# Optimization experiments

Measured on AMD Instinct MI355X. Metric: run time of the kernel, lower is better.

## Reference

```python
import jax, jax.numpy as jnp
import numpy as np
import math

K = 1.0          # Lorentz manifold curvature param: points satisfy <x,x>_L = -K
NUM_HEADS = 16
EPS = 1e-6
B, L, D = 2, 2048, 1024


def lorentz_inner(x, y):
    # <x,y>_L = -x0*y0 + sum_{i>0} xi*yi  (over last dim)
    return jnp.sum(x * y, axis=-1) - 2.0 * x[..., 0] * y[..., 0]


def project_to_lorentz(z):
    # treat z[...,1:] as space components, recompute time so <x,x>_L = -K
    space = z[..., 1:]
    time = jnp.sqrt(K + jnp.sum(space * space, axis=-1, keepdims=True))
    return jnp.concatenate([time, space], axis=-1)


def hlinear(x, W, b, num_heads):
    # Lorentz linear layer (Chen et al. 2022): Euclidean affine map on the
    # ambient coordinates followed by curvature-aware time re-normalization.
    z = x @ W.T + b  # (B, L, D)
    if num_heads > 0:
        Bz, Lz, Dz = z.shape
        z = z.reshape(Bz, Lz, num_heads, Dz // num_heads)  # (B, L, H, dh)
    return project_to_lorentz(z)


def setup_inputs() -> dict:
    key = jax.random.key(0)
    ks = jax.random.split(key, 8)
    def mk_point(k):
        # random manifold points: random space part, valid time coordinate
        z = jax.random.normal(k, (B, L, D), dtype=jnp.float32) * 0.5
        return project_to_lorentz(z)
    scale = 1.0 / math.sqrt(D)
    def mk_w(k):
        return jax.random.normal(k, (D, D), dtype=jnp.float32) * scale
    return {
        "query": mk_point(ks[0]),
        "key": mk_point(ks[1]),
        "value": mk_point(ks[2]),
        "W_Q": mk_w(ks[3]), "b_Q": jnp.zeros((D,), jnp.float32),
        "W_K": mk_w(ks[4]), "b_K": jnp.zeros((D,), jnp.float32),
        "W_V": mk_w(ks[5]), "b_V": jnp.zeros((D,), jnp.float32),
        "W_O": mk_w(ks[6]), "b_O": jnp.zeros((D,), jnp.float32),
    }


def reference(query, key, value, W_Q, b_Q, W_K, b_K, W_V, b_V, W_O, b_O):
    H = NUM_HEADS
    q = hlinear(query, W_Q, b_Q, H)  # (B, L, H, dh) on per-head Lorentz manifold
    k = hlinear(key, W_K, b_K, H)
    v = hlinear(value, W_V, b_V, H)
    dh = q.shape[-1]
    # Lorentzian inner products <q_i, k_j>_L per head: (B, H, Lq, Lk)
    ip = (jnp.einsum('bqhd,bkhd->bhqk', q, k)
          - 2.0 * jnp.einsum('bqh,bkh->bhqk', q[..., 0], k[..., 0]))
    # negative squared Lorentz distance: -d_L^2 = 2K + 2<q,k>_L, scaled by sqrt(dh)
    scores = (2.0 * K + 2.0 * ip) * (1.0 / math.sqrt(dh))
    attn = jax.nn.softmax(scores, axis=-1)
    # Lorentzian centroid aggregation (Law et al.): normalize weighted sum back
    # onto the hyperboloid.
    mu = jnp.einsum('bhqk,bkhd->bqhd', attn, v)  # (B, L, H, dh)
    norm = jnp.sqrt(jnp.maximum(jnp.abs(lorentz_inner(mu, mu)), EPS))
    out_heads = math.sqrt(K) * mu / norm[..., None]
    cat = out_heads.reshape(out_heads.shape[0], out_heads.shape[1], -1)  # (B, L, D)
    return hlinear(cat, W_O, b_O, 0)  # (B, L, D) on the manifold
```

## Files before the change

kernel.cpp:

```cpp
#include <hip/hip_runtime.h>
#include <math.h>

namespace {
constexpr int Ln = 2048;
constexpr int Dn = 1024;
constexpr int Mn = 4096;
constexpr float QSCALE = 0.25f * 1.44269504088896340736f;
}

typedef unsigned short u16;
typedef unsigned int u32;
typedef __attribute__((ext_vector_type(4))) float f32x4;
typedef __attribute__((ext_vector_type(8))) __bf16 bf16x8;
typedef __attribute__((ext_vector_type(4))) unsigned short u16x4;
typedef __attribute__((ext_vector_type(8))) unsigned short u16x8;
typedef __attribute__((ext_vector_type(4))) unsigned int u32x4;


__device__ __forceinline__ u16 f2bf(float f) {
    union { float f; unsigned u; } cv; cv.f = f;
    unsigned u = cv.u + 0x7fffu + ((cv.u >> 16) & 1u);
    return (u16)(u >> 16);
}
__device__ __forceinline__ float bf2f(u16 h) {
    union { unsigned u; float f; } cv; cv.u = ((unsigned)h) << 16;
    return cv.f;
}

__device__ __forceinline__ u32 pkbf(float a, float b) {
    union { __bf16 h[2]; u32 u; } cv;
    cv.h[0] = (__bf16)a; cv.h[1] = (__bf16)b;
    return cv.u;
}

#if __has_builtin(__builtin_amdgcn_exp2f)
__device__ __forceinline__ float exp2_fast(float x) {
    return __builtin_amdgcn_exp2f(x);
}
#else
__device__ __forceinline__ float exp2_fast(float x) {
    float r;
    asm("v_exp_f32 %0, %1" : "=v"(r) : "v"(x));
    return r;
}
#endif

template <int CTRL>
__device__ __forceinline__ float dppf(float x) {
    return __int_as_float(__builtin_amdgcn_update_dpp(
        0, __float_as_int(x), CTRL, 0xf, 0xf, true));
}
__device__ __forceinline__ float red16_add(float x) {
    x += dppf<0xB1>(x);
    x += dppf<0x4E>(x);
    x += dppf<0x141>(x);
    x += dppf<0x140>(x);
    return x;
}

__device__ __forceinline__ void gload16(const void* g, void* l) {
    __builtin_amdgcn_global_load_lds(
        (const __attribute__((address_space(1))) unsigned int*)g,
        (__attribute__((address_space(3))) unsigned int*)l, 16, 0, 0);
}

__global__ __launch_bounds__(256)
void cvt_in3(const float* __restrict__ i0, const float* __restrict__ i1,
             const float* __restrict__ i2,
             u16* __restrict__ o0, u16* __restrict__ o1, u16* __restrict__ o2)
{
    const int z = blockIdx.y;
    const float* in = z == 0 ? i0 : (z == 1 ? i1 : i2);
    u16* out       = z == 0 ? o0 : (z == 1 ? o1 : o2);
    int i = blockIdx.x * 256 + threadIdx.x;
    f32x4 v = ((const f32x4*)in)[i];
    u16x4 o;
#pragma unroll
    for (int j = 0; j < 4; ++j) o[j] = f2bf(v[j]);
    int l = i >> 8;
    int e = (i & 255) * 4;
    int idx = l * 1024 + (e & ~63) + (((((e >> 3) & 7) ^ (l & 7))) << 3) + (e & 7);
    *(u16x4*)&out[idx] = o;
}

__global__ __launch_bounds__(256)
void cvt_w(const float* __restrict__ w0, const float* __restrict__ w1,
           const float* __restrict__ w2, const float* __restrict__ w3,
           u16* __restrict__ q0, u16* __restrict__ q1,
           u16* __restrict__ q2, u16* __restrict__ q3)
{
    const int z = blockIdx.y;
    int i = blockIdx.x * 256 + threadIdx.x;
    if (z < 3) {
        const float* in = z == 0 ? w0 : (z == 1 ? w1 : w2);
        u16* out       = z == 0 ? q0 : (z == 1 ? q1 : q2);
        f32x4 v = ((const f32x4*)in)[i];
        u16x4 o;
#pragma unroll
        for (int j = 0; j < 4; ++j) o[j] = f2bf(v[j]);
        int l = i >> 8;
        int e = (i & 255) * 4;
        int idx = l * 1024 + (e & ~63) + (((((e >> 3) & 7) ^ (l & 7))) << 3) + (e & 7);
        *(u16x4*)&out[idx] = o;
    } else {
        int o  = i >> 8;
        int s0 = (i & 255) * 4;
        int h = s0 >> 6, sl = s0 & 63, a = sl >> 2;
        const float* src = w3 + (size_t)o * 1024 + h * 64;
        u16x4 ov = { f2bf(src[a]), f2bf(src[16 + a]),
                     f2bf(src[32 + a]), f2bf(src[48 + a]) };
        int idx = o * 1024 + h * 64 + (((sl >> 3) ^ (o & 7)) << 3) + (sl & 7);
        *(u16x4*)&q3[idx] = ov;
    }
}

__global__ __launch_bounds__(256)
void gemm_qkv(const u16* __restrict__ xq, const u16* __restrict__ xk,
              const u16* __restrict__ xv, const u16* __restrict__ wq,
              const u16* __restrict__ wk, const u16* __restrict__ wv,
              const float* __restrict__ bq, const float* __restrict__ bk,
              const float* __restrict__ bv,
              u16* __restrict__ oq, u16* __restrict__ ok, u16* __restrict__ ov)
{
    __shared__ u16 As[2][64 * 64];
    __shared__ u16 Bs[2][128 * 64];
    const int t = threadIdx.x;
    const int lane = t & 63, w = t >> 6;
    const int g = lane >> 4, c = lane & 15;
    const int wr = w >> 1, wc = w & 1;
    const int id = blockIdx.x;
    const int bm = ((id & 7) * 8 + ((id >> 3) & 7)) * 64;
    const int bn = ((id >> 6) & 7) * 128;
    const int z  = id >> 9;

    const u16* A = z == 0 ? xq : (z == 1 ? xk : xv);
    const u16* W = z == 0 ? wq : (z == 1 ? wk : wv);
    const float* bias = z == 0 ? bq : (z == 1 ? bk : bv);
    u16* Ct = z == 0 ? oq : (z == 1 ? ok : ov);
    const float scale = z == 0 ? QSCALE : 1.f;
    const float tsign = z == 0 ? -1.f : 1.f;

    f32x4 acc[2][4];
    const f32x4 z4 = {0.f, 0.f, 0.f, 0.f};
#pragma unroll
    for (int i = 0; i < 2; ++i)
#pragma unroll
        for (int j = 0; j < 4; ++j) acc[i][j] = z4;

    const int sr = t >> 3, sb2 = (t & 7) * 8;
    const u16* Ap = A + (size_t)(bm + sr) * Dn + sb2;
    const u16* Wp = W + (size_t)(bn + sr) * Dn + sb2;

    auto stage = [&](int buf, int k0) {
        gload16(Ap + k0,            &As[buf][t * 8]);
        gload16(Ap + 32 * Dn + k0,  &As[buf][(256 + t) * 8]);
        gload16(Wp + k0,            &Bs[buf][t * 8]);
        gload16(Wp + 32 * Dn + k0,  &Bs[buf][(256 + t) * 8]);
        gload16(Wp + 64 * Dn + k0,  &Bs[buf][(512 + t) * 8]);
        gload16(Wp + 96 * Dn + k0,  &Bs[buf][(768 + t) * 8]);
    };

    stage(0, 0);
    for (int ki = 0; ki < 16; ++ki) {
        __syncthreads();
        if (ki + 1 < 16) stage((ki + 1) & 1, (ki + 1) * 64);
        const u16* as = As[ki & 1];
        const u16* bs = Bs[ki & 1];
#pragma unroll
        for (int kk = 0; kk < 2; ++kk) {
            const int so = ((kk * 4 + g) ^ (c & 7)) << 3;
            bf16x8 a[2], b[4];
#pragma unroll
            for (int mi = 0; mi < 2; ++mi)
                a[mi] = *(const bf16x8*)&as[(wr * 32 + mi * 16 + c) * 64 + so];
#pragma unroll
            for (int ni = 0; ni < 4; ++ni)
                b[ni] = *(const bf16x8*)&bs[(wc * 64 + ni * 16 + c) * 64 + so];
            __builtin_amdgcn_s_setprio(1);
#pragma unroll
            for (int mi = 0; mi < 2; ++mi)
#pragma unroll
                for (int ni = 0; ni < 4; ++ni)
                    acc[mi][ni] = __builtin_amdgcn_mfma_f32_16x16x32_bf16(
                        a[mi], b[ni], acc[mi][ni], 0, 0, 0);
            __builtin_amdgcn_s_setprio(0);
        }
    }

    const int hcb = bn + wc * 64;
    const int h = hcb >> 6;
#pragma unroll
    for (int mi = 0; mi < 2; ++mi)
#pragma unroll
        for (int j = 0; j < 4; ++j) {
            int ll = bm + wr * 32 + mi * 16 + g * 4 + j;
            float zv[4];
#pragma unroll
            for (int ni = 0; ni < 4; ++ni)
                zv[ni] = acc[mi][ni][j] + bias[hcb + ni * 16 + c];
            float loc = zv[0]*zv[0] + zv[1]*zv[1] + zv[2]*zv[2] + zv[3]*zv[3];
            if (c == 0) loc -= zv[0] * zv[0];
            loc = red16_add(loc);
            float tval = sqrtf(1.f + loc);
            float v0 = (c == 0) ? tsign * tval : zv[0];
            int bb = ll >> 11, l2 = ll & 2047;
            u16* dst = Ct + (((size_t)bb * 16 + h) * Ln + l2) * 64;
            u16x4 pkv = { f2bf(v0 * scale), f2bf(zv[1] * scale),
                          f2bf(zv[2] * scale), f2bf(zv[3] * scale) };
            *(u16x4*)&dst[(4 * c) ^ ((ll & 7) << 3)] = pkv;
        }
}

__global__ __launch_bounds__(256)
void transpose_v(const u16* __restrict__ vin, u16* __restrict__ vout)
{
    __shared__ u16 raw[64 * 64];
    const int t = threadIdx.x;
    const int bh = blockIdx.x, lc = blockIdx.y;
    const u16* src = vin + ((size_t)bh * Ln + lc * 64) * 64;
#pragma unroll
    for (int p = 0; p < 2; ++p) {
        int ci = p * 256 + t;
        *(u16x8*)&raw[ci * 8] = *(const u16x8*)(src + ci * 8);
    }
    __syncthreads();
    const int d = t >> 2, cp0 = (t & 3) * 16;
    const int s = ((d & 15) << 2) | (d >> 4);
    u16 buf[16];
#pragma unroll
    for (int i = 0; i < 16; ++i) {
        int cp = cp0 + i;
        int n = ((cp >> 5) << 5) | (((cp >> 2) & 1) << 4) | (((cp >> 3) & 3) << 2) | (cp & 3);
        buf[i] = raw[n * 64 + ((((s >> 3) ^ (n & 7)) << 3) | (s & 7))];
    }
    u16* dst = vout + ((size_t)bh * 64 + d) * Ln + lc * 64;
    int b0 = cp0 >> 3;
    *(u16x8*)&dst[((b0 ^ (d & 7)) << 3)]       = *(const u16x8*)&buf[0];
    *(u16x8*)&dst[(((b0 + 1) ^ (d & 7)) << 3)] = *(const u16x8*)&buf[8];
}

__global__ __launch_bounds__(256, 4)
void attn_mfma(const u16* __restrict__ qt, const u16* __restrict__ kt,
               const u16* __restrict__ vT, u16* __restrict__ part)
{
    __shared__ u16 smem[4 * 4096];

    const int t = threadIdx.x;
    const int lane = t & 63, w = t >> 6;
    const int g = lane >> 4, c = lane & 15;
    const int id  = blockIdx.x;
    const int qb  = (id >> 3) & 15;
    const int gidx = (id & 7) | ((id >> 7) << 3);
    const int bh  = gidx & 31;
    const int kvh = gidx >> 5;
    const int q0  = qb * 128;
    const u16* Q = qt + (size_t)bh * Ln * 64;
    const u16* K = kt + (size_t)bh * Ln * 64 + (size_t)kvh * (1024 * 64);
    const u16* V = vT + (size_t)bh * 64 * (size_t)Ln + kvh * 1024;

    bf16x8 qa[2][2];
#pragma unroll
    for (int mi = 0; mi < 2; ++mi)
#pragma unroll
        for (int kk = 0; kk < 2; ++kk) {
            int row = q0 + w * 32 + mi * 16 + c;
            qa[mi][kk] = *(const bf16x8*)(Q + (size_t)row * 64 +
                                          (((kk * 4 + g) ^ (c & 7)) << 3));
        }

    f32x4 o[2][4];
    const f32x4 z4 = {0.f, 0.f, 0.f, 0.f};
#pragma unroll
    for (int mi = 0; mi < 2; ++mi)
#pragma unroll
        for (int di = 0; di < 4; ++di) o[mi][di] = z4;

    const int fb0 = c * 128 + (((0 + g) ^ (c & 7)) << 4);
    const int fb1 = c * 128 + (((4 + g) ^ (c & 7)) << 4);

    char* sb = (char*)smem;
    const int cr = t >> 3, cb = t & 7;
    const u16* kp = K + (size_t)cr * 64 + cb * 8;
    const u16* vp = V + (size_t)cr * Ln + cb * 8;

    gload16(kp,            sb + t * 16);
    gload16(kp + 2048,     sb + 4096 + t * 16);
    gload16(vp,            sb + 16384 + t * 16);
    gload16(vp + 32 * Ln,  sb + 16384 + 4096 + t * 16);

    constexpr int NC = 1024 / 64;
    for (int ch = 0; ch < NC; ++ch) {
        __syncthreads();
        if (ch + 1 < NC) {
            const u16* kn = kp + (ch + 1) * 4096;
            const u16* vn = vp + (ch + 1) * 64;
            char* db = sb + (((ch + 1) & 1) << 13);
            gload16(kn,           db + t * 16);
            gload16(kn + 2048,    db + 4096 + t * 16);
            gload16(vn,           db + 16384 + t * 16);
            gload16(vn + 32 * Ln, db + 16384 + 4096 + t * 16);
        }
        const char* kbb = sb + ((ch & 1) << 13);
        const char* vbb = kbb + 16384;

        f32x4 sf[2][4];
#pragma unroll
        for (int mi = 0; mi < 2; ++mi)
#pragma unroll
            for (int ni = 0; ni < 4; ++ni) sf[mi][ni] = z4;
        __builtin_amdgcn_s_setprio(1);
#pragma unroll
        for (int kk = 0; kk < 2; ++kk) {
            const int fb = kk ? fb1 : fb0;
            bf16x8 kb[4];
#pragma unroll
            for (int ni = 0; ni < 4; ++ni)
                kb[ni] = *(const bf16x8*)(kbb + fb + ni * 2048);
#pragma unroll
            for (int mi = 0; mi < 2; ++mi)
#pragma unroll
                for (int ni = 0; ni < 4; ++ni)
                    sf[mi][ni] = __builtin_amdgcn_mfma_f32_16x16x32_bf16(
                        kb[ni], qa[mi][kk], sf[mi][ni], 0, 0, 0);
        }
        __builtin_amdgcn_s_setprio(0);

        bf16x8 paf[2][2];
#pragma unroll
        for (int mi = 0; mi < 2; ++mi) {
            float ex[4][4];
#pragma unroll
            for (int ni = 0; ni < 4; ++ni)
#pragma unroll
                for (int j = 0; j < 4; ++j)
                    ex[ni][j] = exp2_fast(sf[mi][ni][j]);
            u32x4 p0 = { pkbf(ex[0][0], ex[0][1]), pkbf(ex[0][2], ex[0][3]),
                         pkbf(ex[1][0], ex[1][1]), pkbf(ex[1][2], ex[1][3]) };
            u32x4 p1 = { pkbf(ex[2][0], ex[2][1]), pkbf(ex[2][2], ex[2][3]),
                         pkbf(ex[3][0], ex[3][1]), pkbf(ex[3][2], ex[3][3]) };
            paf[mi][0] = __builtin_bit_cast(bf16x8, p0);
            paf[mi][1] = __builtin_bit_cast(bf16x8, p1);
        }

        __builtin_amdgcn_s_setprio(1);
#pragma unroll
        for (int kk = 0; kk < 2; ++kk) {
            const int fb = kk ? fb1 : fb0;
#pragma unroll
            for (int di = 0; di < 4; ++di) {
                bf16x8 vb = *(const bf16x8*)(vbb + fb + di * 2048);
#pragma unroll
                for (int mi = 0; mi < 2; ++mi)
                    o[mi][di] = __builtin_amdgcn_mfma_f32_16x16x32_bf16(
                        paf[mi][kk], vb, o[mi][di], 0, 0, 0);
            }
        }
        __builtin_amdgcn_s_setprio(0);
    }

    u16* P = part + (size_t)(kvh * 32 + bh) * (4 * 2048 * 16);
#pragma unroll
    for (int mi = 0; mi < 2; ++mi)
#pragma unroll
        for (int j = 0; j < 4; ++j) {
            int row = q0 + w * 32 + mi * 16 + g * 4 + j;
#pragma unroll
            for (int di = 0; di < 4; ++di)
                P[(di * 2048 + row) * 16 + c] = f2bf(o[mi][di][j]);
        }
}

__global__ __launch_bounds__(256)
void attn_combine(const u16* __restrict__ part, u16* __restrict__ cat)
{
    const int grp = blockIdx.x * 16 + (threadIdx.x >> 4);
    const int c = threadIdx.x & 15;
    const int bh = grp >> 11, q = grp & 2047;
    const u16* P0 = part + (size_t)bh * (4 * 2048 * 16);
    const u16* P1 = part + (size_t)(32 + bh) * (4 * 2048 * 16);
    float mu[4];
#pragma unroll
    for (int di = 0; di < 4; ++di) {
        int idx = (di * 2048 + q) * 16 + c;
        mu[di] = bf2f(P0[idx]) + bf2f(P1[idx]);
    }
    float loc = mu[0]*mu[0] + mu[1]*mu[1] + mu[2]*mu[2] + mu[3]*mu[3];
    if (c == 0) loc -= 2.f * mu[0] * mu[0];
    loc = red16_add(loc);
    float rn = rsqrtf(fmaxf(fabsf(loc), 1e-6f));
    const int b = bh >> 4, h = bh & 15;
    u16* dst = cat + ((size_t)b * Ln + q) * Dn + h * 64;
    u16x4 pkv = { f2bf(mu[0] * rn), f2bf(mu[1] * rn),
                  f2bf(mu[2] * rn), f2bf(mu[3] * rn) };
    *(u16x4*)&dst[(4 * c) ^ ((q & 7) << 3)] = pkv;
}

__global__ __launch_bounds__(256)
void gemm_o(const u16* __restrict__ A, const u16* __restrict__ B,
            const float* __restrict__ bias, float* __restrict__ C)
{
    __shared__ u16 As[2][64 * 64];
    __shared__ u16 Bs[2][128 * 64];
    const int t = threadIdx.x;
    const int lane = t & 63, w = t >> 6;
    const int g = lane >> 4, c = lane & 15;
    const int wr = w >> 1, wc = w & 1;
    const int id = blockIdx.x;
    const int bm = ((id & 7) * 8 + ((id >> 3) & 7)) * 64;
    const int bn = (id >> 6) * 128;

    f32x4 acc[2][4];
    const f32x4 z4 = {0.f, 0.f, 0.f, 0.f};
#pragma unroll
    for (int i = 0; i < 2; ++i)
#pragma unroll
        for (int j = 0; j < 4; ++j) acc[i][j] = z4;

    const int sr = t >> 3, sb2 = (t & 7) * 8;
    const u16* Ap = A + (size_t)(bm + sr) * Dn + sb2;
    const u16* Bp = B + (size_t)(bn + sr) * Dn + sb2;

    auto stage = [&](int buf, int k0) {
        gload16(Ap + k0,            &As[buf][t * 8]);
        gload16(Ap + 32 * Dn + k0,  &As[buf][(256 + t) * 8]);
        gload16(Bp + k0,            &Bs[buf][t * 8]);
        gload16(Bp + 32 * Dn + k0,  &Bs[buf][(256 + t) * 8]);
        gload16(Bp + 64 * Dn + k0,  &Bs[buf][(512 + t) * 8]);
        gload16(Bp + 96 * Dn + k0,  &Bs[buf][(768 + t) * 8]);
    };

    stage(0, 0);
    for (int ki = 0; ki < 16; ++ki) {
        __syncthreads();
        if (ki + 1 < 16) stage((ki + 1) & 1, (ki + 1) * 64);
        const u16* as = As[ki & 1];
        const u16* bs = Bs[ki & 1];
#pragma unroll
        for (int kk = 0; kk < 2; ++kk) {
            const int so = ((kk * 4 + g) ^ (c & 7)) << 3;
            bf16x8 a[2], b[4];
#pragma unroll
            for (int mi = 0; mi < 2; ++mi)
                a[mi] = *(const bf16x8*)&as[(wr * 32 + mi * 16 + c) * 64 + so];
#pragma unroll
            for (int ni = 0; ni < 4; ++ni)
                b[ni] = *(const bf16x8*)&bs[(wc * 64 + ni * 16 + c) * 64 + so];
            __builtin_amdgcn_s_setprio(1);
#pragma unroll
            for (int mi = 0; mi < 2; ++mi)
#pragma unroll
                for (int ni = 0; ni < 4; ++ni)
                    acc[mi][ni] = __builtin_amdgcn_mfma_f32_16x16x32_bf16(
                        a[mi], b[ni], acc[mi][ni], 0, 0, 0);
            __builtin_amdgcn_s_setprio(0);
        }
    }

#pragma unroll
    for (int mi = 0; mi < 2; ++mi)
#pragma unroll
        for (int j = 0; j < 4; ++j) {
            size_t row = bm + wr * 32 + mi * 16 + g * 4 + j;
#pragma unroll
            for (int ni = 0; ni < 4; ++ni) {
                int col = bn + wc * 64 + ni * 16 + c;
                C[row * Dn + col] = acc[mi][ni][j] + bias[col];
            }
        }
}

__global__ __launch_bounds__(256)
void lorentz_row_full(float* __restrict__ z)
{
    __shared__ float red[4];
    const int t = threadIdx.x;
    const size_t base = (size_t)blockIdx.x * Dn;
    float4 v = *(const float4*)&z[base + t * 4];
    if (t == 0) v.x = 0.f;
    float ssq = v.x * v.x + v.y * v.y + v.z * v.z + v.w * v.w;
#pragma unroll
    for (int off = 32; off; off >>= 1) ssq += __shfl_xor(ssq, off);
    if ((t & 63) == 0) red[t >> 6] = ssq;
    __syncthreads();
    if (t == 0) z[base] = sqrtf(1.0f + red[0] + red[1] + red[2] + red[3]);
}

extern "C" void kernel_launch(void* const* d_in, const int* in_sizes, int n_in,
                              void* d_out, int out_size, void* d_ws, size_t ws_size,
                              hipStream_t stream)
{
    const float* query = (const float*)d_in[0];
    const float* key_  = (const float*)d_in[1];
    const float* value = (const float*)d_in[2];
    const float* W_Q   = (const float*)d_in[3];
    const float* b_Q   = (const float*)d_in[4];
    const float* W_K   = (const float*)d_in[5];
    const float* b_K   = (const float*)d_in[6];
    const float* W_V   = (const float*)d_in[7];
    const float* b_V   = (const float*)d_in[8];
    const float* W_O   = (const float*)d_in[9];
    const float* b_O   = (const float*)d_in[10];

    const size_t MD = (size_t)Mn * Dn;
    const size_t DD = (size_t)Dn * Dn;
    u16* xq   = (u16*)d_ws;
    u16* xk   = xq + MD;
    u16* xv   = xk + MD;
    u16* wo   = xv + MD;
    u16* q_t  = wo + DD;
    u16* k_t  = q_t + MD;
    u16* wq   = k_t + MD;
    u16* wk   = wq + DD;
    u16* wv   = wk + DD;
    u16* v_ln = wv + DD;
    u16* part = wq;
    u16* v_T  = xv;
    u16* cat  = xk;

    dim3 ci(Mn * Dn / 1024, 3);
    cvt_in3<<<ci, 256, 0, stream>>>(query, key_, value, xq, xk, xv);
    dim3 cw(Dn * Dn / 1024, 4);
    cvt_w<<<cw, 256, 0, stream>>>(W_Q, W_K, W_V, W_O, wq, wk, wv, wo);

    gemm_qkv<<<1536, 256, 0, stream>>>(xq, xk, xv, wq, wk, wv,
                                       b_Q, b_K, b_V, q_t, k_t, v_ln);

    dim3 tg(32, Ln / 64);
    transpose_v<<<tg, 256, 0, stream>>>(v_ln, v_T);

    attn_mfma<<<1024, 256, 0, stream>>>(q_t, k_t, v_T, part);

    attn_combine<<<4096, 256, 0, stream>>>(part, cat);

    gemm_o<<<512, 256, 0, stream>>>(cat, wo, b_O, (float*)d_out);
    lorentz_row_full<<<Mn, 256, 0, stream>>>((float*)d_out);
}
```

Before: 124.3 us.

## Fuse output row sum-of-squares into gemm_o epilogue and merge conversion kernels

Merges the input and weight bf16 conversion kernels into one launch, which also zeroes a per-row sum-of-squares buffer. The output GEMM epilogue now accumulates each row's squared spatial components with DPP reductions and atomicAdds them into that buffer. A tiny kernel then writes the time coordinate from the buffer, so the full re-read of the 16 MB fp32 output is no longer needed. The cost is extra atomics and grid blocks that exit early for the smaller weight conversions.

After: 122.1 us, median of 3. Within noise of the previous version (-1.8%).

```diff
diff --git a/kernel.cpp b/kernel.cpp
--- a/kernel.cpp
+++ b/kernel.cpp
@@ -65,35 +65,40 @@
 }
 
 __global__ __launch_bounds__(256)
-void cvt_in3(const float* __restrict__ i0, const float* __restrict__ i1,
-             const float* __restrict__ i2,
-             u16* __restrict__ o0, u16* __restrict__ o1, u16* __restrict__ o2)
+void cvt_all(const float* __restrict__ i0, const float* __restrict__ i1,
+             const float* __restrict__ i2, const float* __restrict__ w0,
+             const float* __restrict__ w1, const float* __restrict__ w2,
+             const float* __restrict__ w3,
+             u16* __restrict__ o0, u16* __restrict__ o1, u16* __restrict__ o2,
+             u16* __restrict__ q0, u16* __restrict__ q1,
+             u16* __restrict__ q2, u16* __restrict__ q3,
+             float* __restrict__ ssq)
 {
     const int z = blockIdx.y;
-    const float* in = z == 0 ? i0 : (z == 1 ? i1 : i2);
-    u16* out       = z == 0 ? o0 : (z == 1 ? o1 : o2);
-    int i = blockIdx.x * 256 + threadIdx.x;
-    f32x4 v = ((const f32x4*)in)[i];
-    u16x4 o;
-#pragma unroll
-    for (int j = 0; j < 4; ++j) o[j] = f2bf(v[j]);
-    int l = i >> 8;
-    int e = (i & 255) * 4;
-    int idx = l * 1024 + (e & ~63) + (((((e >> 3) & 7) ^ (l & 7))) << 3) + (e & 7);
-    *(u16x4*)&out[idx] = o;
-}
-
-__global__ __launch_bounds__(256)
-void cvt_w(const float* __restrict__ w0, const float* __restrict__ w1,
-           const float* __restrict__ w2, const float* __restrict__ w3,
-           u16* __restrict__ q0, u16* __restrict__ q1,
-           u16* __restrict__ q2, u16* __restrict__ q3)
-{
-    const int z = blockIdx.y;
-    int i = blockIdx.x * 256 + threadIdx.x;
+    const int bx = blockIdx.x;
+    if (z == 0 && bx == 0) {
+        const f32x4 zz = {0.f, 0.f, 0.f, 0.f};
+#pragma unroll
+        for (int j = 0; j < 4; ++j)
+            ((f32x4*)ssq)[threadIdx.x * 4 + j] = zz;
+    }
     if (z < 3) {
-        const float* in = z == 0 ? w0 : (z == 1 ? w1 : w2);
-        u16* out       = z == 0 ? q0 : (z == 1 ? q1 : q2);
+        const float* in = z == 0 ? i0 : (z == 1 ? i1 : i2);
+        u16* out       = z == 0 ? o0 : (z == 1 ? o1 : o2);
+        int i = bx * 256 + threadIdx.x;
+        f32x4 v = ((const f32x4*)in)[i];
+        u16x4 o;
+#pragma unroll
+        for (int j = 0; j < 4; ++j) o[j] = f2bf(v[j]);
+        int l = i >> 8;
+        int e = (i & 255) * 4;
+        int idx = l * 1024 + (e & ~63) + (((((e >> 3) & 7) ^ (l & 7))) << 3) + (e & 7);
+        *(u16x4*)&out[idx] = o;
+    } else if (z < 6) {
+        if (bx >= 1024) return;
+        const float* in = z == 3 ? w0 : (z == 4 ? w1 : w2);
+        u16* out       = z == 3 ? q0 : (z == 4 ? q1 : q2);
+        int i = bx * 256 + threadIdx.x;
         f32x4 v = ((const f32x4*)in)[i];
         u16x4 o;
 #pragma unroll
@@ -103,6 +108,8 @@
         int idx = l * 1024 + (e & ~63) + (((((e >> 3) & 7) ^ (l & 7))) << 3) + (e & 7);
         *(u16x4*)&out[idx] = o;
     } else {
+        if (bx >= 1024) return;
+        int i = bx * 256 + threadIdx.x;
         int o  = i >> 8;
         int s0 = (i & 255) * 4;
         int h = s0 >> 6, sl = s0 & 63, a = sl >> 2;
@@ -397,7 +404,8 @@
 
 __global__ __launch_bounds__(256)
 void gemm_o(const u16* __restrict__ A, const u16* __restrict__ B,
-            const float* __restrict__ bias, float* __restrict__ C)
+            const float* __restrict__ bias, float* __restrict__ C,
+            float* __restrict__ ssq)
 {
     __shared__ u16 As[2][64 * 64];
     __shared__ u16 Bs[2][128 * 64];
@@ -461,28 +469,24 @@
 #pragma unroll
         for (int j = 0; j < 4; ++j) {
             size_t row = bm + wr * 32 + mi * 16 + g * 4 + j;
+            float prt = 0.f;
 #pragma unroll
             for (int ni = 0; ni < 4; ++ni) {
                 int col = bn + wc * 64 + ni * 16 + c;
-                C[row * Dn + col] = acc[mi][ni][j] + bias[col];
+                float v = acc[mi][ni][j] + bias[col];
+                C[row * Dn + col] = v;
+                if (col != 0) prt += v * v;
             }
+            prt = red16_add(prt);
+            if (c == 0) atomicAdd(&ssq[row], prt);
         }
 }
 
 __global__ __launch_bounds__(256)
-void lorentz_row_full(float* __restrict__ z)
-{
-    __shared__ float red[4];
-    const int t = threadIdx.x;
-    const size_t base = (size_t)blockIdx.x * Dn;
-    float4 v = *(const float4*)&z[base + t * 4];
-    if (t == 0) v.x = 0.f;
-    float ssq = v.x * v.x + v.y * v.y + v.z * v.z + v.w * v.w;
-#pragma unroll
-    for (int off = 32; off; off >>= 1) ssq += __shfl_xor(ssq, off);
-    if ((t & 63) == 0) red[t >> 6] = ssq;
-    __syncthreads();
-    if (t == 0) z[base] = sqrtf(1.0f + red[0] + red[1] + red[2] + red[3]);
+void lorentz_fix(float* __restrict__ z, const float* __restrict__ ssq)
+{
+    int row = blockIdx.x * 256 + threadIdx.x;
+    z[(size_t)row * Dn] = sqrtf(1.f + ssq[row]);
 }
 
 extern "C" void kernel_launch(void* const* d_in, const int* in_sizes, int n_in,
@@ -516,11 +520,11 @@
     u16* part = wq;
     u16* v_T  = xv;
     u16* cat  = xk;
-
-    dim3 ci(Mn * Dn / 1024, 3);
-    cvt_in3<<<ci, 256, 0, stream>>>(query, key_, value, xq, xk, xv);
-    dim3 cw(Dn * Dn / 1024, 4);
-    cvt_w<<<cw, 256, 0, stream>>>(W_Q, W_K, W_V, W_O, wq, wk, wv, wo);
+    float* ssq = (float*)((u16*)d_ws + (size_t)30 * 1024 * 1024);
+
+    dim3 ca(Mn * Dn / 1024, 7);
+    cvt_all<<<ca, 256, 0, stream>>>(query, key_, value, W_Q, W_K, W_V, W_O,
+                                    xq, xk, xv, wq, wk, wv, wo, ssq);
 
     gemm_qkv<<<1536, 256, 0, stream>>>(xq, xk, xv, wq, wk, wv,
                                        b_Q, b_K, b_V, q_t, k_t, v_ln);
@@ -532,6 +536,6 @@
 
     attn_combine<<<4096, 256, 0, stream>>>(part, cat);
 
-    gemm_o<<<512, 256, 0, stream>>>(cat, wo, b_O, (float*)d_out);
-    lorentz_row_full<<<Mn, 256, 0, stream>>>((float*)d_out);
-}
+    gemm_o<<<512, 256, 0, stream>>>(cat, wo, b_O, (float*)d_out, ssq);
+    lorentz_fix<<<Mn / 256, 256, 0, stream>>>((float*)d_out, ssq);
+}
```
